# Performance work log

Measured on AMD Instinct MI355X. Metric: run time of the kernel, lower is better.

Reference implementation:

```python
import jax, jax.numpy as jnp
import numpy as np

BETA_MIN = 0.01
BETA_MAX = 0.995
EPS = 1e-6


def setup_inputs() -> dict:
    key = jax.random.key(0)
    k1, k2, k3, k4 = jax.random.split(key, 4)
    B, T, D = 16, 4096, 128
    return {
        "q": jax.random.normal(k1, (B, T, D), dtype=jnp.float32),
        "k": jax.random.normal(k2, (B, T, D), dtype=jnp.float32),
        "v": jax.random.normal(k3, (B, T, D), dtype=jnp.float32),
        "beta": jax.random.uniform(k4, (B, T, 1), dtype=jnp.float32),
        "mask": jnp.ones((B, T, 1), dtype=jnp.float32),
        "base_beta_1": jnp.asarray(2.0, dtype=jnp.float32),
        "base_beta_2": jnp.asarray(3.0, dtype=jnp.float32),
    }


def _delta_scan(q, k, v, beta, mask, base_beta_1, base_beta_2):
    B, T, D = q.shape
    phi_q = jax.nn.elu(q) + 1.0  # positive feature map
    phi_k = jax.nn.elu(k) + 1.0
    b1_base = jnp.clip(jax.nn.sigmoid(base_beta_1), BETA_MIN, BETA_MAX)
    b2_base = jnp.clip(jax.nn.sigmoid(base_beta_2), BETA_MIN, BETA_MAX)

    # time-major for scan: [T, B, ...]
    xs = (
        jnp.swapaxes(phi_q, 0, 1),
        jnp.swapaxes(phi_k, 0, 1),
        jnp.swapaxes(v, 0, 1),
        jnp.swapaxes(beta, 0, 1),
        jnp.swapaxes(mask, 0, 1),
    )

    H1 = jnp.zeros((B, D, D), dtype=q.dtype)
    H2 = jnp.zeros((B, D, D), dtype=q.dtype)
    Z1 = jnp.zeros((B, D), dtype=q.dtype)
    Z2 = jnp.zeros((B, D), dtype=q.dtype)

    def step(carry, x):
        H1, H2, Z1, Z2 = carry
        q_t, k_t, v_t, b_in_t, m_t = x  # q_t:[B,D], b_in_t/m_t:[B,1]
        b_in_t = jnp.clip(b_in_t, BETA_MIN, BETA_MAX)
        b1_t = jnp.clip(b1_base * b_in_t, BETA_MIN, BETA_MAX)  # [B,1]
        b2_t = jnp.clip(b2_base * b_in_t, BETA_MIN, BETA_MAX)
        kv = jnp.einsum('bd,be->bde', k_t, v_t) * m_t[:, :, None]  # masked outer product
        H1 = H1 * b1_t[:, :, None] + kv
        H2 = H2 * b2_t[:, :, None] + kv
        Z1 = Z1 * b1_t + k_t * m_t
        Z2 = Z2 * b2_t + k_t * m_t
        num = jnp.einsum('bd,bde->be', q_t, H1 + H2)
        den = jnp.maximum(jnp.sum(q_t * (Z1 + Z2), axis=-1, keepdims=True), EPS)
        o_t = num / den * m_t
        return (H1, H2, Z1, Z2), o_t

    _, outs = jax.lax.scan(step, (H1, H2, Z1, Z2), xs)
    return jnp.swapaxes(outs, 0, 1)  # [B, T, D]


def reference(q, k, v, beta, mask, base_beta_1, base_beta_2):
    return _delta_scan(q, k, v, beta, mask, base_beta_1, base_beta_2)
```

## Files before the change

### kernel.cpp

```cpp
#include <hip/hip_runtime.h>

#define B_ 16
#define T_ 4096
#define D_ 128
#define L_ 128
#define NC_ 32
#define CH_ (B_*NC_)
#define LDP 136

typedef __attribute__((ext_vector_type(8))) short bf16x8;
typedef __attribute__((ext_vector_type(4))) float f32x4;

__device__ __forceinline__ float clampf(float x, float lo, float hi) {
    return fminf(fmaxf(x, lo), hi);
}
__device__ __forceinline__ float phi_f(float x) {
    return x > 0.f ? x + 1.f : __expf(x);
}
__device__ __forceinline__ unsigned short bf16r(float f) {
    unsigned u = __builtin_bit_cast(unsigned, f);
    u += 0x7FFFu + ((u >> 16) & 1u);
    return (unsigned short)(u >> 16);
}
__device__ __forceinline__ float fbf(unsigned short h) {
    unsigned u = ((unsigned)h) << 16; return __builtin_bit_cast(float, u);
}
__device__ __forceinline__ unsigned pack2bf(float a, float b) {
    return (unsigned)bf16r(a) | ((unsigned)bf16r(b) << 16);
}
__device__ __forceinline__ uint4 pack8(const float* f) {
    uint4 r;
    r.x = pack2bf(f[0], f[1]); r.y = pack2bf(f[2], f[3]);
    r.z = pack2bf(f[4], f[5]); r.w = pack2bf(f[6], f[7]);
    return r;
}
__device__ __forceinline__ f32x4 zero4() { f32x4 z; z[0]=0.f; z[1]=0.f; z[2]=0.f; z[3]=0.f; return z; }

__device__ __forceinline__ int aidx(int row, int k0) {
    return (((row >> 4) * 4 + (k0 >> 5)) * 64 + ((k0 >> 3) & 3) * 16 + (row & 15)) * 8;
}

__global__ void k0w(const float* __restrict__ beta,
                    const float* __restrict__ bb1, const float* __restrict__ bb2,
                    float* __restrict__ lg1, float* __restrict__ lg2,
                    float* __restrict__ wexp) {
    int ch = blockIdx.x;
    int b = ch / NC_, c = ch % NC_;
    int tbase = b * T_ + c * L_;
    int tid = threadIdx.x;
    int lane = tid & 63, w = tid >> 6;
    __shared__ float tot1s[2], tot2s[2];

    float b1b = clampf(1.f / (1.f + __expf(-bb1[0])), 0.01f, 0.995f);
    float b2b = clampf(1.f / (1.f + __expf(-bb2[0])), 0.01f, 0.995f);
    float be = clampf(beta[tbase + tid], 0.01f, 0.995f);
    float x1 = __logf(clampf(b1b * be, 0.01f, 0.995f));
    float x2 = __logf(clampf(b2b * be, 0.01f, 0.995f));
#pragma unroll
    for (int off = 1; off < 64; off <<= 1) {
        float y1 = __shfl_up(x1, off);
        float y2 = __shfl_up(x2, off);
        if (lane >= off) { x1 += y1; x2 += y2; }
    }
    if (lane == 63) { tot1s[w] = x1; tot2s[w] = x2; }
    __syncthreads();
    if (w == 1) { x1 += tot1s[0]; x2 += tot2s[0]; }
    float tot1 = tot1s[0] + tot1s[1];
    float tot2 = tot2s[0] + tot2s[1];
    lg1[tbase + tid] = x1;
    lg2[tbase + tid] = x2;
    wexp[(size_t)ch * 128 + tid]                     = __expf(tot1 - x1);
    wexp[(size_t)CH_ * 128 + (size_t)ch * 128 + tid] = __expf(tot2 - x2);
}

__global__ __launch_bounds__(256) void kS(
        const float* __restrict__ kk, const float* __restrict__ vv,
        const float* __restrict__ mask,
        unsigned short* __restrict__ phiKT, unsigned short* __restrict__ VtT) {
    int g = blockIdx.x;
    int ch = g >> 2, q = g & 3;
    int b = ch / NC_, c = ch % NC_;
    int tbase = b * T_ + c * L_;
    int tid = threadIdx.x;
    size_t cb = (size_t)ch * 16384;

#pragma unroll
    for (int p = 0; p < 2; ++p) {
        int i = p * 256 + tid;
        int s = q * 32 + (i >> 4), d0 = (i & 15) * 8;
        const float* kp = &kk[(size_t)(tbase + s) * D_ + d0];
        float4 x0 = *(const float4*)kp, x1 = *(const float4*)(kp + 4);
        float m = mask[tbase + s];
        float pq[8] = {phi_f(x0.x)*m, phi_f(x0.y)*m, phi_f(x0.z)*m, phi_f(x0.w)*m,
                       phi_f(x1.x)*m, phi_f(x1.y)*m, phi_f(x1.z)*m, phi_f(x1.w)*m};
        *(uint4*)&phiKT[cb + aidx(s, d0)] = pack8(pq);
    }

#pragma unroll
    for (int p = 0; p < 2; ++p) {
        int i = p * 256 + tid;
        int e = q * 32 + (i & 31), s0 = (i >> 5) * 8;
        const float* vp = &vv[(size_t)(tbase + s0) * D_ + e];
        float f[8];
#pragma unroll
        for (int j = 0; j < 8; ++j)
            f[j] = vp[(size_t)j * D_];
        *(uint4*)&VtT[cb + aidx(e, s0)] = pack8(f);
    }
}

__global__ __launch_bounds__(256, 2) void kC(
        const float* __restrict__ kk, const float* __restrict__ mask,
        const unsigned short* __restrict__ VtT, const float* __restrict__ wexp,
        unsigned short* __restrict__ Cws, float* __restrict__ zc) {
    int ch = blockIdx.x;
    int b = ch / NC_, c = ch % NC_;
    int tbase = b * T_ + c * L_;
    int tid = threadIdx.x, lane = tid & 63, w = tid >> 6;
    int l15 = lane & 15, lg4 = lane >> 4;
    size_t cb = (size_t)ch * 16384;
    __shared__ unsigned short sKt[16384];

#pragma unroll
    for (int p = 0; p < 8; ++p) {
        int i = p * 256 + tid;
        int d = i & 127, s0 = (i >> 7) * 8;
        const float* kp = &kk[(size_t)(tbase + s0) * D_ + d];
        const float* mp = &mask[tbase + s0];
        float f[8];
#pragma unroll
        for (int j = 0; j < 8; ++j)
            f[j] = phi_f(kp[(size_t)j * D_]) * mp[j];
        *(uint4*)&sKt[aidx(d, s0)] = pack8(f);
    }
    __syncthreads();

    const float* wp0 = &wexp[(size_t)ch * 128];
    const float* wp1 = &wexp[(size_t)CH_ * 128 + (size_t)ch * 128];

    f32x4 acc[2][2][8];
#pragma unroll
    for (int st = 0; st < 2; ++st)
#pragma unroll
        for (int mm = 0; mm < 2; ++mm)
#pragma unroll
            for (int n = 0; n < 8; ++n) acc[st][mm][n] = zero4();
    float zp[2][8];
#pragma unroll
    for (int st = 0; st < 2; ++st)
#pragma unroll
        for (int n = 0; n < 8; ++n) zp[st][n] = 0.f;

#pragma unroll
    for (int ks = 0; ks < 4; ++ks) {
        int koff = ks * 32 + lg4 * 8;
        float wl0[8], wl1[8];
        {
            float4 a0 = *(const float4*)&wp0[koff];
            float4 a1 = *(const float4*)&wp0[koff + 4];
            float4 b0 = *(const float4*)&wp1[koff];
            float4 b1 = *(const float4*)&wp1[koff + 4];
            wl0[0]=a0.x; wl0[1]=a0.y; wl0[2]=a0.z; wl0[3]=a0.w;
            wl0[4]=a1.x; wl0[5]=a1.y; wl0[6]=a1.z; wl0[7]=a1.w;
            wl1[0]=b0.x; wl1[1]=b0.y; wl1[2]=b0.z; wl1[3]=b0.w;
            wl1[4]=b1.x; wl1[5]=b1.y; wl1[6]=b1.z; wl1[7]=b1.w;
        }
        bf16x8 as0[2], as1[2];
#pragma unroll
        for (int mm = 0; mm < 2; ++mm) {
            bf16x8 vt = *(const bf16x8*)&VtT[cb + (size_t)((((w * 2 + mm) * 4 + ks) * 64 + lane) * 8)];
#pragma unroll
            for (int j = 0; j < 8; ++j) {
                float av = fbf((unsigned short)vt[j]);
                as0[mm][j] = (short)bf16r(av * wl0[j]);
                as1[mm][j] = (short)bf16r(av * wl1[j]);
            }
        }
        bf16x8 bb[8];
#pragma unroll
        for (int n = 0; n < 8; ++n)
            bb[n] = *(const bf16x8*)&sKt[((n * 4 + ks) * 64 + lane) * 8];
        if (w == 0) {
#pragma unroll
            for (int n = 0; n < 8; ++n)
#pragma unroll
                for (int j = 0; j < 8; ++j) {
                    float kv = fbf((unsigned short)bb[n][j]);
                    zp[0][n] += wl0[j] * kv;
                    zp[1][n] += wl1[j] * kv;
                }
        }
#pragma unroll
        for (int n = 0; n < 8; ++n) {
            acc[0][0][n] = __builtin_amdgcn_mfma_f32_16x16x32_bf16(as0[0], bb[n], acc[0][0][n], 0, 0, 0);
            acc[0][1][n] = __builtin_amdgcn_mfma_f32_16x16x32_bf16(as0[1], bb[n], acc[0][1][n], 0, 0, 0);
            acc[1][0][n] = __builtin_amdgcn_mfma_f32_16x16x32_bf16(as1[0], bb[n], acc[1][0][n], 0, 0, 0);
            acc[1][1][n] = __builtin_amdgcn_mfma_f32_16x16x32_bf16(as1[1], bb[n], acc[1][1][n], 0, 0, 0);
        }
    }

    if (w == 0) {
#pragma unroll
        for (int st = 0; st < 2; ++st)
#pragma unroll
            for (int n = 0; n < 8; ++n) {
                float z = zp[st][n];
                z += __shfl_xor(z, 16); z += __shfl_xor(z, 32);
                if (lg4 == 0)
                    zc[((size_t)(st * B_ + b) * NC_ + c) * D_ + n * 16 + l15] = z;
            }
    }

    __syncthreads();
#pragma unroll
    for (int st = 0; st < 2; ++st) {
#pragma unroll
        for (int mm = 0; mm < 2; ++mm)
#pragma unroll
            for (int n = 0; n < 8; ++n)
#pragma unroll
                for (int r = 0; r < 4; ++r) {
                    int e = (w * 2 + mm) * 16 + lg4 * 4 + r;
                    int d = n * 16 + l15;
                    sKt[aidx(e, d & ~7) + (d & 7)] = bf16r(acc[st][mm][n][r]);
                }
        __syncthreads();
        unsigned short* Cp = Cws + ((size_t)(st * B_ + b) * NC_ + c) * (D_ * D_);
#pragma unroll
        for (int p = 0; p < 8; ++p) {
            int i = tid + p * 256;
            *(uint4*)&Cp[(size_t)i * 8] = *(const uint4*)&sKt[i * 8];
        }
        if (st == 0) __syncthreads();
    }
}

__global__ void k2f(unsigned short* __restrict__ Cws, float* __restrict__ zc,
                    const float* __restrict__ lg1, const float* __restrict__ lg2) {
    int g = blockIdx.x * blockDim.x + threadIdx.x;
    if (g < 131072) {
        int st = g >> 16;
        int rem = g & 65535;
        int b = rem >> 12;
        int de = (rem & 4095) * 4;
        const float* lg = st ? lg2 : lg1;
        size_t base = ((size_t)(st * B_ + b) * NC_) * (D_ * D_) + de;
        float run0 = 0.f, run1 = 0.f, run2 = 0.f, run3 = 0.f;
        for (int c = 0; c < NC_; c++) {
            float a = __expf(lg[b * T_ + c * L_ + L_ - 1]);
            uint2 val = *(uint2*)&Cws[base + (size_t)c * (D_ * D_)];
            float t0 = fbf((unsigned short)(val.x & 0xffff)), t1 = fbf((unsigned short)(val.x >> 16));
            float t2 = fbf((unsigned short)(val.y & 0xffff)), t3 = fbf((unsigned short)(val.y >> 16));
            uint2 wv; wv.x = pack2bf(run0, run1); wv.y = pack2bf(run2, run3);
            *(uint2*)&Cws[base + (size_t)c * (D_ * D_)] = wv;
            run0 = a * run0 + t0; run1 = a * run1 + t1;
            run2 = a * run2 + t2; run3 = a * run3 + t3;
        }
    } else {
        int gz = g - 131072;
        int st = gz >> 11;
        int rem = gz & 2047;
        int b = rem >> 7;
        int d = rem & 127;
        const float* lg = st ? lg2 : lg1;
        size_t base = ((size_t)(st * B_ + b) * NC_) * D_ + d;
        float run = 0.f;
        for (int c = 0; c < NC_; c++) {
            float a = __expf(lg[b * T_ + c * L_ + L_ - 1]);
            float tmp = zc[base + (size_t)c * D_];
            zc[base + (size_t)c * D_] = run;
            run = a * run + tmp;
        }
    }
}

__global__ __launch_bounds__(256, 2) void k3_v6(
        const float* __restrict__ qq, const float* __restrict__ mask,
        const float* __restrict__ lg1, const float* __restrict__ lg2,
        const unsigned short* __restrict__ phiKT, const unsigned short* __restrict__ VtT,
        const unsigned short* __restrict__ Cws, const float* __restrict__ zc,
        float* __restrict__ out) {
    __shared__ unsigned short bufP[4][32 * LDP];
    int ch = blockIdx.x;
    int b = ch / NC_, c = ch % NC_;
    int tbase = b * T_ + c * L_;
    int tid = threadIdx.x, lane = tid & 63, w = tid >> 6;
    int l15 = lane & 15, lg4 = lane >> 4;
    unsigned short* bufPw = &bufP[w][0];
    size_t cb = (size_t)ch * 16384;

    int trow0 = w * 16 + l15, trow1 = 64 + trow0;
    size_t gt0 = (size_t)(tbase + trow0), gt1 = (size_t)(tbase + trow1);

    float lg1t0 = lg1[gt0], lg2t0 = lg2[gt0], mt0 = mask[gt0];
    float lg1t1 = lg1[gt1], lg2t1 = lg2[gt1], mt1 = mask[gt1];
    float a1t0 = __expf(lg1t0), a2t0 = __expf(lg2t0);
    float a1t1 = __expf(lg1t1), a2t1 = __expf(lg2t1);

    bf16x8 qf0[4], qf1[4];
#pragma unroll
    for (int ks = 0; ks < 4; ++ks) {
        int koff = ks * 32 + lg4 * 8;
        const float* qp0 = &qq[gt0 * D_ + koff];
        const float* qp1 = &qq[gt1 * D_ + koff];
        float4 x0 = *(const float4*)qp0, x1 = *(const float4*)(qp0 + 4);
        float4 y0 = *(const float4*)qp1, y1 = *(const float4*)(qp1 + 4);
        float p0[8] = {phi_f(x0.x), phi_f(x0.y), phi_f(x0.z), phi_f(x0.w),
                       phi_f(x1.x), phi_f(x1.y), phi_f(x1.z), phi_f(x1.w)};
        float p1[8] = {phi_f(y0.x), phi_f(y0.y), phi_f(y0.z), phi_f(y0.w),
                       phi_f(y1.x), phi_f(y1.y), phi_f(y1.z), phi_f(y1.w)};
#pragma unroll
        for (int j = 0; j < 8; ++j) {
            qf0[ks][j] = (short)bf16r(p0[j]);
            qf1[ks][j] = (short)bf16r(p1[j]);
        }
    }

    const float* z1p = &zc[((size_t)(0 * B_ + b) * NC_ + c) * D_];
    const float* z2p = &zc[((size_t)(1 * B_ + b) * NC_ + c) * D_];
    float d1_0 = 0.f, d2_0 = 0.f, d1_1 = 0.f, d2_1 = 0.f;
#pragma unroll
    for (int ks = 0; ks < 4; ++ks) {
        int off = ks * 32 + lg4 * 8;
        float4 za = *(const float4*)(z1p + off), zb = *(const float4*)(z1p + off + 4);
        float4 zca = *(const float4*)(z2p + off), zcb = *(const float4*)(z2p + off + 4);
        float z1a[8] = {za.x, za.y, za.z, za.w, zb.x, zb.y, zb.z, zb.w};
        float z2a[8] = {zca.x, zca.y, zca.z, zca.w, zcb.x, zcb.y, zcb.z, zcb.w};
#pragma unroll
        for (int j = 0; j < 8; ++j) {
            float fq0 = fbf((unsigned short)qf0[ks][j]);
            float fq1 = fbf((unsigned short)qf1[ks][j]);
            d1_0 += fq0 * z1a[j]; d2_0 += fq0 * z2a[j];
            d1_1 += fq1 * z1a[j]; d2_1 += fq1 * z2a[j];
        }
    }
    d1_0 += __shfl_xor(d1_0, 16); d1_0 += __shfl_xor(d1_0, 32);
    d2_0 += __shfl_xor(d2_0, 16); d2_0 += __shfl_xor(d2_0, 32);
    d1_1 += __shfl_xor(d1_1, 16); d1_1 += __shfl_xor(d1_1, 32);
    d2_1 += __shfl_xor(d2_1, 16); d2_1 += __shfl_xor(d2_1, 32);

    float rs0 = 0.f, rs1 = 0.f;
#pragma unroll
    for (int mh = 0; mh < 2; ++mh) {
        bf16x8 kf[16];
#pragma unroll
        for (int mm = 0; mm < 4; ++mm)
#pragma unroll
            for (int ks = 0; ks < 4; ++ks)
                kf[mm * 4 + ks] = *(const bf16x8*)&phiKT[cb + (size_t)(((((mh * 4 + mm) * 4) + ks) * 64 + lane) * 8)];
        f32x4 acc0[4], acc1[4];
#pragma unroll
        for (int mm = 0; mm < 4; ++mm) { acc0[mm] = zero4(); acc1[mm] = zero4(); }
#pragma unroll
        for (int ks = 0; ks < 4; ++ks)
#pragma unroll
            for (int mm = 0; mm < 4; ++mm) {
                if (mh == 0)
                    acc0[mm] = __builtin_amdgcn_mfma_f32_16x16x32_bf16(kf[mm * 4 + ks], qf0[ks], acc0[mm], 0, 0, 0);
                acc1[mm] = __builtin_amdgcn_mfma_f32_16x16x32_bf16(kf[mm * 4 + ks], qf1[ks], acc1[mm], 0, 0, 0);
            }
#pragma unroll
        for (int mm = 0; mm < 4; ++mm) {
            int s0 = (mh * 4 + mm) * 16 + lg4 * 4;
            float4 l1s = *(const float4*)&lg1[tbase + s0];
            float4 l2s = *(const float4*)&lg2[tbase + s0];
            float l1a[4] = {l1s.x, l1s.y, l1s.z, l1s.w};
            float l2a[4] = {l2s.x, l2s.y, l2s.z, l2s.w};
            if (mh == 0) {
                float pv[4];
#pragma unroll
                for (int r = 0; r < 4; ++r) {
                    int s = s0 + r;
                    float p = 0.f;
                    if (s <= trow0)
                        p = acc0[mm][r] * (__expf(lg1t0 - l1a[r]) + __expf(lg2t0 - l2a[r]));
                    pv[r] = p; rs0 += p;
                }
                uint2 dd; dd.x = pack2bf(pv[0], pv[1]); dd.y = pack2bf(pv[2], pv[3]);
                *(uint2*)&bufPw[l15 * LDP + s0] = dd;
            }
            {
                float pv[4];
#pragma unroll
                for (int r = 0; r < 4; ++r) {
                    int s = s0 + r;
                    float p = 0.f;
                    if (s <= trow1)
                        p = acc1[mm][r] * (__expf(lg1t1 - l1a[r]) + __expf(lg2t1 - l2a[r]));
                    pv[r] = p; rs1 += p;
                }
                uint2 dd; dd.x = pack2bf(pv[0], pv[1]); dd.y = pack2bf(pv[2], pv[3]);
                *(uint2*)&bufPw[(16 + l15) * LDP + s0] = dd;
            }
        }
    }
    rs0 += __shfl_xor(rs0, 16); rs0 += __shfl_xor(rs0, 32);
    rs1 += __shfl_xor(rs1, 16); rs1 += __shfl_xor(rs1, 32);
    float osc0 = mt0 / fmaxf(a1t0 * d1_0 + a2t0 * d2_0 + rs0, 1e-6f);
    float osc1 = mt1 / fmaxf(a1t1 * d1_1 + a2t1 * d2_1 + rs1, 1e-6f);

    f32x4 acc_o0[8], acc_o1[8];
#pragma unroll
    for (int m = 0; m < 8; ++m) { acc_o0[m] = zero4(); acc_o1[m] = zero4(); }
#pragma unroll
    for (int st = 0; st < 2; ++st) {
        const unsigned short* Hp = Cws + ((size_t)(st * B_ + b) * NC_ + c) * (D_ * D_);
        float sc0 = st ? a2t0 : a1t0;
        float sc1 = st ? a2t1 : a1t1;
#pragma unroll
        for (int ks2 = 0; ks2 < 2; ++ks2) {
            bf16x8 hf[16];
#pragma unroll
            for (int kq = 0; kq < 2; ++kq)
#pragma unroll
                for (int m = 0; m < 8; ++m)
                    hf[kq * 8 + m] = *(const bf16x8*)&Hp[(size_t)(((m * 4 + ks2 * 2 + kq) * 64 + lane) * 8)];
#pragma unroll
            for (int kq = 0; kq < 2; ++kq) {
                int ks = ks2 * 2 + kq;
                bf16x8 qs0, qs1;
#pragma unroll
                for (int j = 0; j < 8; ++j) {
                    qs0[j] = (short)bf16r(fbf((unsigned short)qf0[ks][j]) * sc0);
                    qs1[j] = (short)bf16r(fbf((unsigned short)qf1[ks][j]) * sc1);
                }
#pragma unroll
                for (int m = 0; m < 8; ++m) {
                    acc_o0[m] = __builtin_amdgcn_mfma_f32_16x16x32_bf16(hf[kq * 8 + m], qs0, acc_o0[m], 0, 0, 0);
                    acc_o1[m] = __builtin_amdgcn_mfma_f32_16x16x32_bf16(hf[kq * 8 + m], qs1, acc_o1[m], 0, 0, 0);
                }
            }
        }
    }

#pragma unroll
    for (int ks = 0; ks < 4; ++ks) {
        bf16x8 vf[8];
#pragma unroll
        for (int m = 0; m < 8; ++m)
            vf[m] = *(const bf16x8*)&VtT[cb + (size_t)(((m * 4 + ks) * 64 + lane) * 8)];
        bf16x8 pf1 = *(const bf16x8*)&bufPw[(16 + l15) * LDP + ks * 32 + lg4 * 8];
        if (ks < 2) {
            bf16x8 pf0 = *(const bf16x8*)&bufPw[l15 * LDP + ks * 32 + lg4 * 8];
#pragma unroll
            for (int m = 0; m < 8; ++m)
                acc_o0[m] = __builtin_amdgcn_mfma_f32_16x16x32_bf16(vf[m], pf0, acc_o0[m], 0, 0, 0);
        }
#pragma unroll
        for (int m = 0; m < 8; ++m)
            acc_o1[m] = __builtin_amdgcn_mfma_f32_16x16x32_bf16(vf[m], pf1, acc_o1[m], 0, 0, 0);
    }

#pragma unroll
    for (int m = 0; m < 8; ++m) {
        float4 o0, o1;
        o0.x = acc_o0[m][0] * osc0; o0.y = acc_o0[m][1] * osc0;
        o0.z = acc_o0[m][2] * osc0; o0.w = acc_o0[m][3] * osc0;
        o1.x = acc_o1[m][0] * osc1; o1.y = acc_o1[m][1] * osc1;
        o1.z = acc_o1[m][2] * osc1; o1.w = acc_o1[m][3] * osc1;
        *(float4*)&out[gt0 * D_ + m * 16 + lg4 * 4] = o0;
        *(float4*)&out[gt1 * D_ + m * 16 + lg4 * 4] = o1;
    }
}

extern "C" void kernel_launch(void* const* d_in, const int* in_sizes, int n_in,
                              void* d_out, int out_size, void* d_ws, size_t ws_size,
                              hipStream_t stream) {
    const float* q    = (const float*)d_in[0];
    const float* k    = (const float*)d_in[1];
    const float* v    = (const float*)d_in[2];
    const float* beta = (const float*)d_in[3];
    const float* mask = (const float*)d_in[4];
    const float* bb1  = (const float*)d_in[5];
    const float* bb2  = (const float*)d_in[6];
    float* out = (float*)d_out;

    size_t n_lg = (size_t)B_ * T_;
    size_t n_z  = (size_t)2 * B_ * NC_ * D_;
    size_t n_w  = (size_t)2 * CH_ * 128;
    size_t n_C  = (size_t)2 * B_ * NC_ * D_ * D_;
    size_t n_kt = (size_t)B_ * T_ * D_;
    size_t need = (2 * n_lg + n_z + n_w) * sizeof(float) + (n_C + 2 * n_kt) * sizeof(unsigned short);
    if (ws_size < need) return;

    float* lg1  = (float*)d_ws;
    float* lg2  = lg1 + n_lg;
    float* zc   = lg2 + n_lg;
    float* wexp = zc + n_z;
    unsigned short* Cws    = (unsigned short*)(wexp + n_w);
    unsigned short* phiKT  = Cws + n_C;
    unsigned short* VtT    = phiKT + n_kt;

    k0w<<<CH_, 128, 0, stream>>>(beta, bb1, bb2, lg1, lg2, wexp);
    kS<<<4 * CH_, 256, 0, stream>>>(k, v, mask, phiKT, VtT);
    kC<<<CH_, 256, 0, stream>>>(k, mask, VtT, wexp, Cws, zc);
    k2f<<<528, 256, 0, stream>>>(Cws, zc, lg1, lg2);
    k3_v6<<<CH_, 256, 0, stream>>>(q, mask, lg1, lg2, phiKT, VtT, Cws, zc, out);
}
```

Baseline: 89.74 us.

## Split output kernel to 8 waves with one 16-row tile each and causal skip

The final chunk-output kernel now launches 512 threads per chunk, and each wave handles a single 16-row query tile instead of two. Each wave computes only the causal key blocks it needs (loop bounds depend on the wave index), which trims the intra-chunk score and PV work. The aim is more waves in flight to hide global-load latency on the H/K/V fragment reads. In exchange, per-thread register headroom drops under the 512,4 launch bounds, and loads of the shared H and V tiles are now repeated across more waves.

```diff
diff --git a/kernel.cpp b/kernel.cpp
--- a/kernel.cpp
+++ b/kernel.cpp
@@ -274,13 +274,13 @@
     }
 }
 
-__global__ __launch_bounds__(256, 2) void k3_v6(
+__global__ __launch_bounds__(512, 4) void k3_v7(
         const float* __restrict__ qq, const float* __restrict__ mask,
         const float* __restrict__ lg1, const float* __restrict__ lg2,
         const unsigned short* __restrict__ phiKT, const unsigned short* __restrict__ VtT,
         const unsigned short* __restrict__ Cws, const float* __restrict__ zc,
         float* __restrict__ out) {
-    __shared__ unsigned short bufP[4][32 * LDP];
+    __shared__ unsigned short bufP[8][16 * LDP];
     int ch = blockIdx.x;
     int b = ch / NC_, c = ch % NC_;
     int tbase = b * T_ + c * L_;
@@ -289,36 +289,27 @@
     unsigned short* bufPw = &bufP[w][0];
     size_t cb = (size_t)ch * 16384;
 
-    int trow0 = w * 16 + l15, trow1 = 64 + trow0;
-    size_t gt0 = (size_t)(tbase + trow0), gt1 = (size_t)(tbase + trow1);
-
-    float lg1t0 = lg1[gt0], lg2t0 = lg2[gt0], mt0 = mask[gt0];
-    float lg1t1 = lg1[gt1], lg2t1 = lg2[gt1], mt1 = mask[gt1];
-    float a1t0 = __expf(lg1t0), a2t0 = __expf(lg2t0);
-    float a1t1 = __expf(lg1t1), a2t1 = __expf(lg2t1);
-
-    bf16x8 qf0[4], qf1[4];
+    int trow = w * 16 + l15;
+    size_t gt = (size_t)(tbase + trow);
+
+    float lg1t = lg1[gt], lg2t = lg2[gt], mt = mask[gt];
+    float a1t = __expf(lg1t), a2t = __expf(lg2t);
+
+    bf16x8 qf[4];
 #pragma unroll
     for (int ks = 0; ks < 4; ++ks) {
         int koff = ks * 32 + lg4 * 8;
-        const float* qp0 = &qq[gt0 * D_ + koff];
-        const float* qp1 = &qq[gt1 * D_ + koff];
-        float4 x0 = *(const float4*)qp0, x1 = *(const float4*)(qp0 + 4);
-        float4 y0 = *(const float4*)qp1, y1 = *(const float4*)(qp1 + 4);
+        const float* qp = &qq[gt * D_ + koff];
+        float4 x0 = *(const float4*)qp, x1 = *(const float4*)(qp + 4);
         float p0[8] = {phi_f(x0.x), phi_f(x0.y), phi_f(x0.z), phi_f(x0.w),
                        phi_f(x1.x), phi_f(x1.y), phi_f(x1.z), phi_f(x1.w)};
-        float p1[8] = {phi_f(y0.x), phi_f(y0.y), phi_f(y0.z), phi_f(y0.w),
-                       phi_f(y1.x), phi_f(y1.y), phi_f(y1.z), phi_f(y1.w)};
-#pragma unroll
-        for (int j = 0; j < 8; ++j) {
-            qf0[ks][j] = (short)bf16r(p0[j]);
-            qf1[ks][j] = (short)bf16r(p1[j]);
-        }
+#pragma unroll
+        for (int j = 0; j < 8; ++j) qf[ks][j] = (short)bf16r(p0[j]);
     }
 
     const float* z1p = &zc[((size_t)(0 * B_ + b) * NC_ + c) * D_];
     const float* z2p = &zc[((size_t)(1 * B_ + b) * NC_ + c) * D_];
-    float d1_0 = 0.f, d2_0 = 0.f, d1_1 = 0.f, d2_1 = 0.f;
+    float d1 = 0.f, d2 = 0.f;
 #pragma unroll
     for (int ks = 0; ks < 4; ++ks) {
         int off = ks * 32 + lg4 * 8;
@@ -328,138 +319,93 @@
         float z2a[8] = {zca.x, zca.y, zca.z, zca.w, zcb.x, zcb.y, zcb.z, zcb.w};
 #pragma unroll
         for (int j = 0; j < 8; ++j) {
-            float fq0 = fbf((unsigned short)qf0[ks][j]);
-            float fq1 = fbf((unsigned short)qf1[ks][j]);
-            d1_0 += fq0 * z1a[j]; d2_0 += fq0 * z2a[j];
-            d1_1 += fq1 * z1a[j]; d2_1 += fq1 * z2a[j];
-        }
-    }
-    d1_0 += __shfl_xor(d1_0, 16); d1_0 += __shfl_xor(d1_0, 32);
-    d2_0 += __shfl_xor(d2_0, 16); d2_0 += __shfl_xor(d2_0, 32);
-    d1_1 += __shfl_xor(d1_1, 16); d1_1 += __shfl_xor(d1_1, 32);
-    d2_1 += __shfl_xor(d2_1, 16); d2_1 += __shfl_xor(d2_1, 32);
-
-    float rs0 = 0.f, rs1 = 0.f;
-#pragma unroll
-    for (int mh = 0; mh < 2; ++mh) {
-        bf16x8 kf[16];
-#pragma unroll
-        for (int mm = 0; mm < 4; ++mm)
+            float fq = fbf((unsigned short)qf[ks][j]);
+            d1 += fq * z1a[j]; d2 += fq * z2a[j];
+        }
+    }
+    d1 += __shfl_xor(d1, 16); d1 += __shfl_xor(d1, 32);
+    d2 += __shfl_xor(d2, 16); d2 += __shfl_xor(d2, 32);
+
+    int SN = (w | 1) + 1;
+    int KP = SN >> 1;
+    float rs = 0.f;
+    for (int sp = 0; sp < KP; ++sp) {
+        bf16x8 kf[8];
+#pragma unroll
+        for (int mm = 0; mm < 2; ++mm)
 #pragma unroll
             for (int ks = 0; ks < 4; ++ks)
-                kf[mm * 4 + ks] = *(const bf16x8*)&phiKT[cb + (size_t)(((((mh * 4 + mm) * 4) + ks) * 64 + lane) * 8)];
-        f32x4 acc0[4], acc1[4];
-#pragma unroll
-        for (int mm = 0; mm < 4; ++mm) { acc0[mm] = zero4(); acc1[mm] = zero4(); }
+                kf[mm * 4 + ks] = *(const bf16x8*)&phiKT[cb + (size_t)(((((sp * 2 + mm) * 4) + ks) * 64 + lane) * 8)];
+        f32x4 accs[2];
+        accs[0] = zero4(); accs[1] = zero4();
 #pragma unroll
         for (int ks = 0; ks < 4; ++ks)
 #pragma unroll
-            for (int mm = 0; mm < 4; ++mm) {
-                if (mh == 0)
-                    acc0[mm] = __builtin_amdgcn_mfma_f32_16x16x32_bf16(kf[mm * 4 + ks], qf0[ks], acc0[mm], 0, 0, 0);
-                acc1[mm] = __builtin_amdgcn_mfma_f32_16x16x32_bf16(kf[mm * 4 + ks], qf1[ks], acc1[mm], 0, 0, 0);
-            }
-#pragma unroll
-        for (int mm = 0; mm < 4; ++mm) {
-            int s0 = (mh * 4 + mm) * 16 + lg4 * 4;
+            for (int mm = 0; mm < 2; ++mm)
+                accs[mm] = __builtin_amdgcn_mfma_f32_16x16x32_bf16(kf[mm * 4 + ks], qf[ks], accs[mm], 0, 0, 0);
+#pragma unroll
+        for (int mm = 0; mm < 2; ++mm) {
+            int s0 = (sp * 2 + mm) * 16 + lg4 * 4;
             float4 l1s = *(const float4*)&lg1[tbase + s0];
             float4 l2s = *(const float4*)&lg2[tbase + s0];
             float l1a[4] = {l1s.x, l1s.y, l1s.z, l1s.w};
             float l2a[4] = {l2s.x, l2s.y, l2s.z, l2s.w};
-            if (mh == 0) {
-                float pv[4];
-#pragma unroll
-                for (int r = 0; r < 4; ++r) {
-                    int s = s0 + r;
-                    float p = 0.f;
-                    if (s <= trow0)
-                        p = acc0[mm][r] * (__expf(lg1t0 - l1a[r]) + __expf(lg2t0 - l2a[r]));
-                    pv[r] = p; rs0 += p;
-                }
-                uint2 dd; dd.x = pack2bf(pv[0], pv[1]); dd.y = pack2bf(pv[2], pv[3]);
-                *(uint2*)&bufPw[l15 * LDP + s0] = dd;
+            float pv[4];
+#pragma unroll
+            for (int r = 0; r < 4; ++r) {
+                int s = s0 + r;
+                float p = 0.f;
+                if (s <= trow)
+                    p = accs[mm][r] * (__expf(lg1t - l1a[r]) + __expf(lg2t - l2a[r]));
+                pv[r] = p; rs += p;
             }
-            {
-                float pv[4];
-#pragma unroll
-                for (int r = 0; r < 4; ++r) {
-                    int s = s0 + r;
-                    float p = 0.f;
-                    if (s <= trow1)
-                        p = acc1[mm][r] * (__expf(lg1t1 - l1a[r]) + __expf(lg2t1 - l2a[r]));
-                    pv[r] = p; rs1 += p;
-                }
-                uint2 dd; dd.x = pack2bf(pv[0], pv[1]); dd.y = pack2bf(pv[2], pv[3]);
-                *(uint2*)&bufPw[(16 + l15) * LDP + s0] = dd;
-            }
-        }
-    }
-    rs0 += __shfl_xor(rs0, 16); rs0 += __shfl_xor(rs0, 32);
-    rs1 += __shfl_xor(rs1, 16); rs1 += __shfl_xor(rs1, 32);
-    float osc0 = mt0 / fmaxf(a1t0 * d1_0 + a2t0 * d2_0 + rs0, 1e-6f);
-    float osc1 = mt1 / fmaxf(a1t1 * d1_1 + a2t1 * d2_1 + rs1, 1e-6f);
-
-    f32x4 acc_o0[8], acc_o1[8];
-#pragma unroll
-    for (int m = 0; m < 8; ++m) { acc_o0[m] = zero4(); acc_o1[m] = zero4(); }
+            uint2 dd; dd.x = pack2bf(pv[0], pv[1]); dd.y = pack2bf(pv[2], pv[3]);
+            *(uint2*)&bufPw[l15 * LDP + s0] = dd;
+        }
+    }
+    rs += __shfl_xor(rs, 16); rs += __shfl_xor(rs, 32);
+    float osc = mt / fmaxf(a1t * d1 + a2t * d2 + rs, 1e-6f);
+
+    f32x4 acc_o[8];
+#pragma unroll
+    for (int m = 0; m < 8; ++m) acc_o[m] = zero4();
 #pragma unroll
     for (int st = 0; st < 2; ++st) {
         const unsigned short* Hp = Cws + ((size_t)(st * B_ + b) * NC_ + c) * (D_ * D_);
-        float sc0 = st ? a2t0 : a1t0;
-        float sc1 = st ? a2t1 : a1t1;
-#pragma unroll
-        for (int ks2 = 0; ks2 < 2; ++ks2) {
-            bf16x8 hf[16];
-#pragma unroll
-            for (int kq = 0; kq < 2; ++kq)
-#pragma unroll
-                for (int m = 0; m < 8; ++m)
-                    hf[kq * 8 + m] = *(const bf16x8*)&Hp[(size_t)(((m * 4 + ks2 * 2 + kq) * 64 + lane) * 8)];
-#pragma unroll
-            for (int kq = 0; kq < 2; ++kq) {
-                int ks = ks2 * 2 + kq;
-                bf16x8 qs0, qs1;
-#pragma unroll
-                for (int j = 0; j < 8; ++j) {
-                    qs0[j] = (short)bf16r(fbf((unsigned short)qf0[ks][j]) * sc0);
-                    qs1[j] = (short)bf16r(fbf((unsigned short)qf1[ks][j]) * sc1);
-                }
-#pragma unroll
-                for (int m = 0; m < 8; ++m) {
-                    acc_o0[m] = __builtin_amdgcn_mfma_f32_16x16x32_bf16(hf[kq * 8 + m], qs0, acc_o0[m], 0, 0, 0);
-                    acc_o1[m] = __builtin_amdgcn_mfma_f32_16x16x32_bf16(hf[kq * 8 + m], qs1, acc_o1[m], 0, 0, 0);
-                }
-            }
-        }
-    }
-
-#pragma unroll
-    for (int ks = 0; ks < 4; ++ks) {
+        float sc = st ? a2t : a1t;
+#pragma unroll
+        for (int ks = 0; ks < 4; ++ks) {
+            bf16x8 hf[8];
+#pragma unroll
+            for (int m = 0; m < 8; ++m)
+                hf[m] = *(const bf16x8*)&Hp[(size_t)(((m * 4 + ks) * 64 + lane) * 8)];
+            bf16x8 qs;
+#pragma unroll
+            for (int j = 0; j < 8; ++j)
+                qs[j] = (short)bf16r(fbf((unsigned short)qf[ks][j]) * sc);
+#pragma unroll
+            for (int m = 0; m < 8; ++m)
+                acc_o[m] = __builtin_amdgcn_mfma_f32_16x16x32_bf16(hf[m], qs, acc_o[m], 0, 0, 0);
+        }
+    }
+
+    for (int ks = 0; ks < KP; ++ks) {
         bf16x8 vf[8];
 #pragma unroll
         for (int m = 0; m < 8; ++m)
             vf[m] = *(const bf16x8*)&VtT[cb + (size_t)(((m * 4 + ks) * 64 + lane) * 8)];
-        bf16x8 pf1 = *(const bf16x8*)&bufPw[(16 + l15) * LDP + ks * 32 + lg4 * 8];
-        if (ks < 2) {
-            bf16x8 pf0 = *(const bf16x8*)&bufPw[l15 * LDP + ks * 32 + lg4 * 8];
-#pragma unroll
-            for (int m = 0; m < 8; ++m)
-                acc_o0[m] = __builtin_amdgcn_mfma_f32_16x16x32_bf16(vf[m], pf0, acc_o0[m], 0, 0, 0);
-        }
+        bf16x8 pf = *(const bf16x8*)&bufPw[l15 * LDP + ks * 32 + lg4 * 8];
 #pragma unroll
         for (int m = 0; m < 8; ++m)
-            acc_o1[m] = __builtin_amdgcn_mfma_f32_16x16x32_bf16(vf[m], pf1, acc_o1[m], 0, 0, 0);
+            acc_o[m] = __builtin_amdgcn_mfma_f32_16x16x32_bf16(vf[m], pf, acc_o[m], 0, 0, 0);
     }
 
 #pragma unroll
     for (int m = 0; m < 8; ++m) {
-        float4 o0, o1;
-        o0.x = acc_o0[m][0] * osc0; o0.y = acc_o0[m][1] * osc0;
-        o0.z = acc_o0[m][2] * osc0; o0.w = acc_o0[m][3] * osc0;
-        o1.x = acc_o1[m][0] * osc1; o1.y = acc_o1[m][1] * osc1;
-        o1.z = acc_o1[m][2] * osc1; o1.w = acc_o1[m][3] * osc1;
-        *(float4*)&out[gt0 * D_ + m * 16 + lg4 * 4] = o0;
-        *(float4*)&out[gt1 * D_ + m * 16 + lg4 * 4] = o1;
+        float4 o;
+        o.x = acc_o[m][0] * osc; o.y = acc_o[m][1] * osc;
+        o.z = acc_o[m][2] * osc; o.w = acc_o[m][3] * osc;
+        *(float4*)&out[gt * D_ + m * 16 + lg4 * 4] = o;
     }
 }
 
@@ -495,5 +441,5 @@
     kS<<<4 * CH_, 256, 0, stream>>>(k, v, mask, phiKT, VtT);
     kC<<<CH_, 256, 0, stream>>>(k, mask, VtT, wexp, Cws, zc);
     k2f<<<528, 256, 0, stream>>>(Cws, zc, lg1, lg2);
-    k3_v6<<<CH_, 256, 0, stream>>>(q, mask, lg1, lg2, phiKT, VtT, Cws, zc, out);
-}
+    k3_v7<<<CH_, 512, 0, stream>>>(q, mask, lg1, lg2, phiKT, VtT, Cws, zc, out);
+}
```

Measured after the change: 89.98 us. About the same (+0.3%).
